# Kernel optimization log

Hardware: AMD Instinct MI355X
Metric: run time of the kernel (lower is better)

Reference implementation:

```python
import jax, jax.numpy as jnp
import numpy as np

N_NODES = 100000


def _gcn_conv(x, src, dst, ew, W, b, n_nodes):
    # PyG GCNConv: x' = D^{-1/2} (A + I) D^{-1/2} (x W) + b, with edge weights.
    h = x @ W  # [N, out]
    deg = jax.ops.segment_sum(ew, dst, num_segments=n_nodes)  # weighted in-degree
    dinv = jnp.where(deg > 0, jax.lax.rsqrt(deg), 0.0)
    norm = dinv[src] * ew * dinv[dst]  # [E]
    msg = h[src] * norm[:, None]  # gather + scale
    out = jax.ops.segment_sum(msg, dst, num_segments=n_nodes)  # scatter-add
    return out + b


def setup_inputs() -> dict:
    key = jax.random.key(0)
    ks = jax.random.split(key, 10)
    E = 1600000
    D_IN, H1, H2, D_OUT = 512, 128, 64, 1
    x = jax.random.normal(ks[0], (N_NODES, D_IN), dtype=jnp.float32)
    edge_index = jax.random.randint(ks[1], (2, E), 0, N_NODES, dtype=jnp.int64)
    edge_attr = jax.random.uniform(ks[2], (E,), dtype=jnp.float32)
    def glorot(k, fan_in, fan_out):
        s = jnp.sqrt(6.0 / (fan_in + fan_out))
        return jax.random.uniform(k, (fan_in, fan_out), minval=-s, maxval=s, dtype=jnp.float32)
    return {
        "x": x,
        "edge_index": edge_index,
        "edge_attr": edge_attr,
        "W1": glorot(ks[3], D_IN, H1), "b1": jnp.zeros((H1,), jnp.float32),
        "W2": glorot(ks[4], H1, H2), "b2": jnp.zeros((H2,), jnp.float32),
        "W3": glorot(ks[5], H2, D_OUT), "b3": jnp.zeros((D_OUT,), jnp.float32),
    }


def reference(x, edge_index, edge_attr, W1, b1, W2, b2, W3, b3):
    n = x.shape[0]
    # add self-loops with weight 1 (PyG GCNConv default)
    loops = jnp.arange(n, dtype=edge_index.dtype)
    src = jnp.concatenate([edge_index[0], loops])
    dst = jnp.concatenate([edge_index[1], loops])
    ew = jnp.concatenate([edge_attr, jnp.ones((n,), edge_attr.dtype)])
    h = _gcn_conv(x, src, dst, ew, W1, b1, n)
    h = jax.nn.relu(h)  # dropout is identity in eval mode
    h = _gcn_conv(h, src, dst, ew, W2, b2, n)
    h = jax.nn.relu(h)
    out = _gcn_conv(h, src, dst, ew, W3, b3, n)
    return out
```

## Files before the change

kernel.cpp:

```cpp
#include <hip/hip_runtime.h>

typedef __attribute__((ext_vector_type(4))) float f32x4;
typedef __attribute__((ext_vector_type(8))) short bf16x8;
typedef __attribute__((ext_vector_type(4))) unsigned short u16x4;

__device__ __forceinline__ unsigned short f2bf(float f) {
  unsigned int u = __builtin_bit_cast(unsigned int, f);
  u += 0x7fffu + ((u >> 16) & 1u);
  return (unsigned short)(u >> 16);
}
__device__ __forceinline__ float bf2f(unsigned short h) {
  unsigned int u = ((unsigned int)h) << 16;
  return __builtin_bit_cast(float, u);
}
__device__ __forceinline__ float bflo(unsigned int u) { return bf2f((unsigned short)(u & 0xffffu)); }
__device__ __forceinline__ float bfhi(unsigned int u) { return bf2f((unsigned short)(u >> 16)); }
__device__ __forceinline__ unsigned int packbf(float a, float b) {
  return (unsigned int)f2bf(a) | ((unsigned int)f2bf(b) << 16);
}

__global__ void hist_rank_k(const int* __restrict__ dst, int* __restrict__ cnt,
                            int* __restrict__ rank, int E) {
  int e = blockIdx.x * blockDim.x + threadIdx.x;
  if (e < E) rank[e] = atomicAdd(&cnt[dst[e]], 1);
}

__global__ void scan1_k(const int* __restrict__ cnt, int* __restrict__ row,
                        int* __restrict__ bsum, int N) {
  __shared__ int sh[256];
  const int tid = threadIdx.x;
  const int base = blockIdx.x * 2048 + tid * 8;
  int v[8]; int s = 0;
#pragma unroll
  for (int i = 0; i < 8; ++i) {
    int idx = base + i;
    v[i] = (idx < N) ? cnt[idx] : 0;
    s += v[i];
  }
  sh[tid] = s;
  __syncthreads();
  for (int off = 1; off < 256; off <<= 1) {
    int t = (tid >= off) ? sh[tid - off] : 0;
    __syncthreads();
    sh[tid] += t;
    __syncthreads();
  }
  int excl = sh[tid] - s;
  if (tid == 255) bsum[blockIdx.x] = sh[255];
  int run = excl;
#pragma unroll
  for (int i = 0; i < 8; ++i) {
    int idx = base + i;
    if (idx < N) row[idx] = run;
    run += v[i];
  }
}
__global__ void scan23_k(int* __restrict__ row, const int* __restrict__ bsum, int N, int E) {
  __shared__ int pref;
  const int seg = (int)((blockIdx.x * blockDim.x) >> 11);
  if (threadIdx.x == 0) {
    int s = 0;
    for (int i = 0; i < seg; ++i) s += bsum[i];
    pref = s;
  }
  __syncthreads();
  int idx = blockIdx.x * blockDim.x + threadIdx.x;
  if (idx < N) row[idx] += pref;
  if (idx == N) row[N] = E;
}
__global__ void scatter_nr_k(const int* __restrict__ src, const int* __restrict__ dst,
                             const float* __restrict__ ew, const int* __restrict__ row,
                             const int* __restrict__ rank, uint2* __restrict__ eadj, int E) {
  int e = blockIdx.x * blockDim.x + threadIdx.x;
  if (e >= E) return;
  int pos = row[dst[e]] + rank[e];
  eadj[pos] = make_uint2((unsigned)src[e], __builtin_bit_cast(unsigned, ew[e]));
}
__global__ void deg_dinv_k(const int* __restrict__ row, const uint2* __restrict__ eadj,
                           float* __restrict__ dinv, int N) {
  int n = blockIdx.x * blockDim.x + threadIdx.x;
  if (n >= N) return;
  float s = 1.0f;
  int end = row[n + 1];
  for (int e = row[n]; e < end; ++e) s += __builtin_bit_cast(float, eadj[e].y);
  dinv[n] = rsqrtf(s);
}
__global__ void conv_wt2_k(const float* __restrict__ W1, unsigned short* __restrict__ Wt1,
                           const float* __restrict__ W2, unsigned short* __restrict__ Wt2) {
  int idx = blockIdx.x * blockDim.x + threadIdx.x;
  if (idx < 512 * 128) {
    int n = idx >> 9, k = idx & 511;
    Wt1[idx] = f2bf(W1[k * 128 + n]);
  } else {
    int j = idx - 512 * 128;
    if (j < 128 * 64) {
      int n = j >> 7, k = j & 127;
      Wt2[j] = f2bf(W2[k * 64 + n]);
    }
  }
}

template<int NC, int KD>
__launch_bounds__(256, 2)
__global__ void gemm_f32a_k(const float* __restrict__ A, const unsigned short* __restrict__ Wt,
                            unsigned short* __restrict__ Hb, int M) {
  constexpr int BM = 128, BK = 64;
  constexpr int WN = 64;
  constexpr int WGN = NC / WN;
  constexpr int WGM = 4 / WGN;
  constexpr int WM = BM / WGM;
  constexpr int FM = WM / 16;
  constexpr int FN = WN / 16;
  constexpr int KSUB = BK / 32;
  constexpr int A_PER_T = BM * (BK / 4) / 256;
  constexpr int B_PER_T = NC * (BK / 8) / 256;
  constexpr int nT = KD / BK;

  __shared__ unsigned short As[BM * BK];
  __shared__ unsigned short Bs[NC * BK];
  char* asb = reinterpret_cast<char*>(As);
  char* bsb = reinterpret_cast<char*>(Bs);

  const int tid = threadIdx.x;
  const int lane = tid & 63;
  const int wid = tid >> 6;
  const int wr = wid / WGN;
  const int wc = wid % WGN;
  const int lg = lane >> 4;
  const int lr = lane & 15;
  const int blockM = blockIdx.x * BM;

  float4 areg[A_PER_T];
  uint4 breg[B_PER_T];

  auto load_tiles = [&](int k0) {
#pragma unroll
    for (int i = 0; i < A_PER_T; ++i) {
      int chunk = tid + i * 256;
      int r = chunk >> 4, c4 = chunk & 15;
      int gr = blockM + r; if (gr >= M) gr = M - 1;
      areg[i] = *reinterpret_cast<const float4*>(A + (size_t)gr * KD + k0 + c4 * 4);
    }
#pragma unroll
    for (int i = 0; i < B_PER_T; ++i) {
      int chunk = tid + i * 256;
      int n = chunk >> 3, c = chunk & 7;
      breg[i] = *reinterpret_cast<const uint4*>(Wt + (size_t)n * KD + k0 + c * 8);
    }
  };

  f32x4 acc[FM][FN] = {};
  load_tiles(0);

  for (int t = 0; t < nT; ++t) {
    __syncthreads();
#pragma unroll
    for (int i = 0; i < A_PER_T; ++i) {
      int chunk = tid + i * 256;
      int r = chunk >> 4, c4 = chunk & 15;
      float4 v = areg[i];
      u16x4 p = { f2bf(v.x), f2bf(v.y), f2bf(v.z), f2bf(v.w) };
      int byte = r * (BK * 2) + ((c4 * 8) ^ ((r & 7) << 4));
      *reinterpret_cast<u16x4*>(asb + byte) = p;
    }
#pragma unroll
    for (int i = 0; i < B_PER_T; ++i) {
      int chunk = tid + i * 256;
      int n = chunk >> 3, c = chunk & 7;
      int byte = n * (BK * 2) + ((c * 16) ^ ((n & 7) << 4));
      *reinterpret_cast<uint4*>(bsb + byte) = breg[i];
    }
    __syncthreads();
    if (t + 1 < nT) load_tiles((t + 1) * BK);

    bf16x8 af[FM][KSUB], bfr[FN][KSUB];
#pragma unroll
    for (int fm = 0; fm < FM; ++fm)
#pragma unroll
      for (int kk = 0; kk < KSUB; ++kk) {
        int row = wr * WM + fm * 16 + lr;
        int k = kk * 32 + lg * 8;
        int byte = row * (BK * 2) + ((k * 2) ^ ((row & 7) << 4));
        af[fm][kk] = *reinterpret_cast<const bf16x8*>(asb + byte);
      }
#pragma unroll
    for (int fn = 0; fn < FN; ++fn)
#pragma unroll
      for (int kk = 0; kk < KSUB; ++kk) {
        int n = wc * WN + fn * 16 + lr;
        int k = kk * 32 + lg * 8;
        int byte = n * (BK * 2) + ((k * 2) ^ ((n & 7) << 4));
        bfr[fn][kk] = *reinterpret_cast<const bf16x8*>(bsb + byte);
      }
#pragma unroll
    for (int kk = 0; kk < KSUB; ++kk)
#pragma unroll
      for (int fm = 0; fm < FM; ++fm)
#pragma unroll
        for (int fn = 0; fn < FN; ++fn)
          acc[fm][fn] = __builtin_amdgcn_mfma_f32_16x16x32_bf16(
              af[fm][kk], bfr[fn][kk], acc[fm][fn], 0, 0, 0);
  }

#pragma unroll
  for (int fm = 0; fm < FM; ++fm)
#pragma unroll
    for (int fn = 0; fn < FN; ++fn) {
      int col = wc * WN + fn * 16 + lr;
#pragma unroll
      for (int j = 0; j < 4; ++j) {
        int row = blockM + wr * WM + fm * 16 + lg * 4 + j;
        if (row < M)
          Hb[(size_t)row * NC + col] = f2bf(acc[fm][fn][j]);
      }
    }
}

__launch_bounds__(256, 2)
__global__ void gemm_bf16a_k(const unsigned short* __restrict__ A,
                             const unsigned short* __restrict__ Wt,
                             unsigned short* __restrict__ Hb, int M) {
  constexpr int BM = 128, BK = 64, NC = 64, KD = 128;
  constexpr int WM = 32;
  constexpr int FM = 2, FN = 4, KSUB = 2;
  constexpr int A_PER_T = 4;
  constexpr int B_PER_T = 2;
  constexpr int nT = KD / BK;

  __shared__ unsigned short As[BM * BK];
  __shared__ unsigned short Bs[NC * BK];
  char* asb = reinterpret_cast<char*>(As);
  char* bsb = reinterpret_cast<char*>(Bs);

  const int tid = threadIdx.x;
  const int lane = tid & 63;
  const int wid = tid >> 6;
  const int lg = lane >> 4;
  const int lr = lane & 15;
  const int blockM = blockIdx.x * BM;

  uint4 areg[A_PER_T];
  uint4 breg[B_PER_T];

  auto load_tiles = [&](int k0) {
#pragma unroll
    for (int i = 0; i < A_PER_T; ++i) {
      int chunk = tid + i * 256;
      int r = chunk >> 3, c = chunk & 7;
      int gr = blockM + r; if (gr >= M) gr = M - 1;
      areg[i] = *reinterpret_cast<const uint4*>(A + (size_t)gr * KD + k0 + c * 8);
    }
#pragma unroll
    for (int i = 0; i < B_PER_T; ++i) {
      int chunk = tid + i * 256;
      int n = chunk >> 3, c = chunk & 7;
      breg[i] = *reinterpret_cast<const uint4*>(Wt + (size_t)n * KD + k0 + c * 8);
    }
  };

  f32x4 acc[FM][FN] = {};
  load_tiles(0);

  for (int t = 0; t < nT; ++t) {
    __syncthreads();
#pragma unroll
    for (int i = 0; i < A_PER_T; ++i) {
      int chunk = tid + i * 256;
      int r = chunk >> 3, c = chunk & 7;
      int byte = r * (BK * 2) + ((c * 16) ^ ((r & 7) << 4));
      *reinterpret_cast<uint4*>(asb + byte) = areg[i];
    }
#pragma unroll
    for (int i = 0; i < B_PER_T; ++i) {
      int chunk = tid + i * 256;
      int n = chunk >> 3, c = chunk & 7;
      int byte = n * (BK * 2) + ((c * 16) ^ ((n & 7) << 4));
      *reinterpret_cast<uint4*>(bsb + byte) = breg[i];
    }
    __syncthreads();
    if (t + 1 < nT) load_tiles((t + 1) * BK);

    bf16x8 af[FM][KSUB], bfr[FN][KSUB];
#pragma unroll
    for (int fm = 0; fm < FM; ++fm)
#pragma unroll
      for (int kk = 0; kk < KSUB; ++kk) {
        int row = wid * WM + fm * 16 + lr;
        int k = kk * 32 + lg * 8;
        int byte = row * (BK * 2) + ((k * 2) ^ ((row & 7) << 4));
        af[fm][kk] = *reinterpret_cast<const bf16x8*>(asb + byte);
      }
#pragma unroll
    for (int fn = 0; fn < FN; ++fn)
#pragma unroll
      for (int kk = 0; kk < KSUB; ++kk) {
        int n = fn * 16 + lr;
        int k = kk * 32 + lg * 8;
        int byte = n * (BK * 2) + ((k * 2) ^ ((n & 7) << 4));
        bfr[fn][kk] = *reinterpret_cast<const bf16x8*>(bsb + byte);
      }
#pragma unroll
    for (int kk = 0; kk < KSUB; ++kk)
#pragma unroll
      for (int fm = 0; fm < FM; ++fm)
#pragma unroll
        for (int fn = 0; fn < FN; ++fn)
          acc[fm][fn] = __builtin_amdgcn_mfma_f32_16x16x32_bf16(
              af[fm][kk], bfr[fn][kk], acc[fm][fn], 0, 0, 0);
  }

#pragma unroll
  for (int fm = 0; fm < FM; ++fm)
#pragma unroll
    for (int fn = 0; fn < FN; ++fn) {
      int col = fn * 16 + lr;
#pragma unroll
      for (int j = 0; j < 4; ++j) {
        int row = blockM + wid * WM + fm * 16 + lg * 4 + j;
        if (row < M)
          Hb[(size_t)row * NC + col] = f2bf(acc[fm][fn][j]);
      }
    }
}

__global__ void agg_csr128_k(const int* __restrict__ row, const uint2* __restrict__ eadj,
                             const unsigned short* __restrict__ h, const float* __restrict__ bias,
                             const float* __restrict__ dinv, unsigned int* __restrict__ o1b, int N) {
  const int lane = threadIdx.x & 63;
  const int node = blockIdx.x * (blockDim.x >> 6) + (threadIdx.x >> 6);
  if (node >= N) return;
  const unsigned int* hu = reinterpret_cast<const unsigned int*>(h);
  const int beg = row[node], end = row[node + 1];
  const float di = dinv[node];
  const float di2 = di * di;
  unsigned int hv = hu[(size_t)node * 64 + lane];
  float acc0 = bflo(hv) * di2;
  float acc1 = bfhi(hv) * di2;
  int e = beg;
  for (; e + 8 <= end; e += 8) {
    uint2 m[8]; float dv[8]; unsigned int hh[8];
#pragma unroll
    for (int i = 0; i < 8; ++i) m[i] = eadj[e + i];
#pragma unroll
    for (int i = 0; i < 8; ++i) dv[i] = dinv[m[i].x];
#pragma unroll
    for (int i = 0; i < 8; ++i) hh[i] = hu[(size_t)m[i].x * 64 + lane];
#pragma unroll
    for (int i = 0; i < 8; ++i) {
      float nm = __builtin_bit_cast(float, m[i].y) * dv[i] * di;
      acc0 += bflo(hh[i]) * nm;
      acc1 += bfhi(hh[i]) * nm;
    }
  }
  for (; e < end; ++e) {
    uint2 m = eadj[e];
    float nm = __builtin_bit_cast(float, m.y) * dinv[m.x] * di;
    unsigned int h0 = hu[(size_t)m.x * 64 + lane];
    acc0 += bflo(h0) * nm;
    acc1 += bfhi(h0) * nm;
  }
  float2 b = reinterpret_cast<const float2*>(bias)[lane];
  float r0 = fmaxf(acc0 + b.x, 0.f);
  float r1 = fmaxf(acc1 + b.y, 0.f);
  o1b[(size_t)node * 64 + lane] = packbf(r0, r1);
}

__global__ void agg_l23_k(const int* __restrict__ row, const uint2* __restrict__ eadj,
                          const unsigned short* __restrict__ h2, const float* __restrict__ b2,
                          const float* __restrict__ W3, const float* __restrict__ dinv,
                          float* __restrict__ h3, int N) {
  const int lane = threadIdx.x & 63;
  const int half = lane >> 5;
  const int l = lane & 31;
  const int node = blockIdx.x * (blockDim.x >> 6) + (threadIdx.x >> 6);
  if (node >= N) return;
  const unsigned int* hu = reinterpret_cast<const unsigned int*>(h2);
  const int beg = row[node], end = row[node + 1];
  const float di = dinv[node];
  float acc0, acc1;
  {
    unsigned int hv = hu[(size_t)node * 32 + l];
    float di2 = (half == 0) ? di * di : 0.f;
    acc0 = bflo(hv) * di2;
    acc1 = bfhi(hv) * di2;
  }
  int e = beg + half;
  for (; e + 6 < end; e += 8) {
    uint2 m[4]; float dv[4]; unsigned int hh[4];
#pragma unroll
    for (int i = 0; i < 4; ++i) m[i] = eadj[e + 2 * i];
#pragma unroll
    for (int i = 0; i < 4; ++i) dv[i] = dinv[m[i].x];
#pragma unroll
    for (int i = 0; i < 4; ++i) hh[i] = hu[(size_t)m[i].x * 32 + l];
#pragma unroll
    for (int i = 0; i < 4; ++i) {
      float nm = __builtin_bit_cast(float, m[i].y) * dv[i] * di;
      acc0 += bflo(hh[i]) * nm;
      acc1 += bfhi(hh[i]) * nm;
    }
  }
  for (; e < end; e += 2) {
    uint2 m = eadj[e];
    float nm = __builtin_bit_cast(float, m.y) * dinv[m.x] * di;
    unsigned int hv = hu[(size_t)m.x * 32 + l];
    acc0 += bflo(hv) * nm;
    acc1 += bfhi(hv) * nm;
  }
  acc0 += __shfl_xor(acc0, 32, 64);
  acc1 += __shfl_xor(acc1, 32, 64);
  float2 bb = reinterpret_cast<const float2*>(b2)[l];
  float2 w3 = reinterpret_cast<const float2*>(W3)[l];
  float v = fmaxf(acc0 + bb.x, 0.f) * w3.x + fmaxf(acc1 + bb.y, 0.f) * w3.y;
#pragma unroll
  for (int off = 16; off > 0; off >>= 1) v += __shfl_xor(v, off, 64);
  if (lane == 0) h3[node] = v;
}

__global__ void agg_csr1_k(const int* __restrict__ row, const uint2* __restrict__ eadj,
                           const float* __restrict__ h3, const float* __restrict__ b3,
                           const float* __restrict__ dinv, float* __restrict__ out, int N) {
  int n = blockIdx.x * blockDim.x + threadIdx.x;
  if (n >= N) return;
  float di = dinv[n];
  float acc = h3[n] * di * di;
  const int beg = row[n], end = row[n + 1];
  int e = beg;
  for (; e + 4 <= end; e += 4) {
    uint2 m[4]; float dv[4]; float hv[4];
#pragma unroll
    for (int i = 0; i < 4; ++i) m[i] = eadj[e + i];
#pragma unroll
    for (int i = 0; i < 4; ++i) dv[i] = dinv[m[i].x];
#pragma unroll
    for (int i = 0; i < 4; ++i) hv[i] = h3[m[i].x];
#pragma unroll
    for (int i = 0; i < 4; ++i)
      acc += hv[i] * (__builtin_bit_cast(float, m[i].y) * dv[i] * di);
  }
  for (; e < end; ++e) {
    uint2 m = eadj[e];
    float nm = __builtin_bit_cast(float, m.y) * dinv[m.x] * di;
    acc += h3[m.x] * nm;
  }
  out[n] = acc + b3[0];
}

extern "C" void kernel_launch(void* const* d_in, const int* in_sizes, int n_in,
                              void* d_out, int out_size, void* d_ws, size_t ws_size,
                              hipStream_t stream) {
  const float* x  = (const float*)d_in[0];
  const int*   ei = (const int*)d_in[1];
  const float* ea = (const float*)d_in[2];
  const float* W1 = (const float*)d_in[3];
  const float* b1 = (const float*)d_in[4];
  const float* W2 = (const float*)d_in[5];
  const float* b2 = (const float*)d_in[6];
  const float* W3 = (const float*)d_in[7];
  const float* b3 = (const float*)d_in[8];
  float* out = (float*)d_out;

  const int N = in_sizes[0] / 512;
  const int E = in_sizes[2];
  const int* src = ei;
  const int* dst = ei + E;

  char* w = (char*)d_ws;
  auto alloc = [&](size_t bytes) {
    char* p = w; w += (bytes + 511) & ~(size_t)511; return p;
  };
  float* dinv         = (float*)alloc((size_t)N * 4);
  int*   cnt          = (int*)alloc((size_t)N * 4);
  int*   rowp         = (int*)alloc((size_t)(N + 1) * 4);
  int*   bsum         = (int*)alloc(4096 * 4);
  int*   rank         = (int*)alloc((size_t)E * 4);
  uint2* eadj         = (uint2*)alloc((size_t)E * 8);
  unsigned short* h1  = (unsigned short*)alloc((size_t)N * 128 * 2);
  unsigned int* o1b   = (unsigned int*)alloc((size_t)N * 64 * 4);
  unsigned short* h2  = (unsigned short*)alloc((size_t)N * 64 * 2);
  float* h3           = (float*)alloc((size_t)N * 4);
  unsigned short* wt1 = (unsigned short*)alloc(512 * 128 * 2);
  unsigned short* wt2 = (unsigned short*)alloc(128 * 64 * 2);

  const int TB = 256;
  const int nb_scan = (N + 2047) / 2048;

  hipMemsetAsync(cnt, 0, (size_t)N * 4, stream);

  hist_rank_k<<<(E + TB - 1) / TB, TB, 0, stream>>>(dst, cnt, rank, E);
  scan1_k<<<nb_scan, 256, 0, stream>>>(cnt, rowp, bsum, N);
  scan23_k<<<(N + 1 + TB - 1) / TB, TB, 0, stream>>>(rowp, bsum, N, E);
  scatter_nr_k<<<(E + TB - 1) / TB, TB, 0, stream>>>(src, dst, ea, rowp, rank, eadj, E);
  deg_dinv_k<<<(N + TB - 1) / TB, TB, 0, stream>>>(rowp, eadj, dinv, N);
  conv_wt2_k<<<(512 * 128 + 128 * 64 + TB - 1) / TB, TB, 0, stream>>>(W1, wt1, W2, wt2);

  const int gblocks = (N + 127) / 128;
  const int ablocks = (N + 3) / 4;
  gemm_f32a_k<128, 512><<<gblocks, TB, 0, stream>>>(x, wt1, h1, N);
  agg_csr128_k<<<ablocks, TB, 0, stream>>>(rowp, eadj, h1, b1, dinv, o1b, N);
  gemm_bf16a_k<<<gblocks, TB, 0, stream>>>((const unsigned short*)o1b, wt2, h2, N);
  agg_l23_k<<<ablocks, TB, 0, stream>>>(rowp, eadj, h2, b2, W3, dinv, h3, N);
  agg_csr1_k<<<(N + TB - 1) / TB, TB, 0, stream>>>(rowp, eadj, h3, b3, dinv, out, N);
}
```

Baseline: 640.0 us.

## Build CSR via two-level bucket partition and prescale features by source dinv

Replaces the per-edge atomic histogram, multi-kernel scan and random scatter CSR build with a two-level scheme. Edges are partitioned into 128-node buckets, then each bucket is sorted in shared memory, which also yields rowp and dinv directly. Separately, the source-side D^{-1/2} factor is folded into the GEMM epilogues and the layer-3 output, so the aggregation kernels no longer gather dinv[src] per edge. Risks: buckets with more than 4096 edges are silently truncated, and packing the source index into 17 bits limits N to 131072.

```diff
diff --git a/kernel.cpp b/kernel.cpp
--- a/kernel.cpp
+++ b/kernel.cpp
@@ -19,22 +19,31 @@
   return (unsigned int)f2bf(a) | ((unsigned int)f2bf(b) << 16);
 }
 
-__global__ void hist_rank_k(const int* __restrict__ dst, int* __restrict__ cnt,
-                            int* __restrict__ rank, int E) {
-  int e = blockIdx.x * blockDim.x + threadIdx.x;
-  if (e < E) rank[e] = atomicAdd(&cnt[dst[e]], 1);
-}
-
-__global__ void scan1_k(const int* __restrict__ cnt, int* __restrict__ row,
-                        int* __restrict__ bsum, int N) {
+#define CHUNK 8192
+
+__global__ void bkt_count_k(const int* __restrict__ dst, int* __restrict__ gcount,
+                            int E, int nbkt) {
+  __shared__ int hist[1024];
+  for (int i = threadIdx.x; i < nbkt; i += 256) hist[i] = 0;
+  __syncthreads();
+  const int base = blockIdx.x * CHUNK;
+  const int cend = min(base + CHUNK, E);
+  for (int e = base + threadIdx.x; e < cend; e += 256)
+    atomicAdd(&hist[dst[e] >> 7], 1);
+  __syncthreads();
+  for (int b = threadIdx.x; b < nbkt; b += 256)
+    if (hist[b]) atomicAdd(&gcount[b], hist[b]);
+}
+
+__global__ void bkt_scan_k(const int* __restrict__ gcount, int* __restrict__ gbase,
+                           int* __restrict__ gcursor, int nbkt) {
   __shared__ int sh[256];
   const int tid = threadIdx.x;
-  const int base = blockIdx.x * 2048 + tid * 8;
-  int v[8]; int s = 0;
-#pragma unroll
-  for (int i = 0; i < 8; ++i) {
-    int idx = base + i;
-    v[i] = (idx < N) ? cnt[idx] : 0;
+  int v[4]; int s = 0;
+#pragma unroll
+  for (int i = 0; i < 4; ++i) {
+    int idx = tid * 4 + i;
+    v[i] = (idx < nbkt) ? gcount[idx] : 0;
     s += v[i];
   }
   sh[tid] = s;
@@ -45,46 +54,97 @@
     sh[tid] += t;
     __syncthreads();
   }
-  int excl = sh[tid] - s;
-  if (tid == 255) bsum[blockIdx.x] = sh[255];
-  int run = excl;
-#pragma unroll
-  for (int i = 0; i < 8; ++i) {
-    int idx = base + i;
-    if (idx < N) row[idx] = run;
+  int run = sh[tid] - s;
+#pragma unroll
+  for (int i = 0; i < 4; ++i) {
+    int idx = tid * 4 + i;
+    if (idx < nbkt) { gbase[idx] = run; gcursor[idx] = run; }
     run += v[i];
   }
 }
-__global__ void scan23_k(int* __restrict__ row, const int* __restrict__ bsum, int N, int E) {
-  __shared__ int pref;
-  const int seg = (int)((blockIdx.x * blockDim.x) >> 11);
-  if (threadIdx.x == 0) {
-    int s = 0;
-    for (int i = 0; i < seg; ++i) s += bsum[i];
-    pref = s;
-  }
-  __syncthreads();
-  int idx = blockIdx.x * blockDim.x + threadIdx.x;
-  if (idx < N) row[idx] += pref;
-  if (idx == N) row[N] = E;
-}
-__global__ void scatter_nr_k(const int* __restrict__ src, const int* __restrict__ dst,
-                             const float* __restrict__ ew, const int* __restrict__ row,
-                             const int* __restrict__ rank, uint2* __restrict__ eadj, int E) {
-  int e = blockIdx.x * blockDim.x + threadIdx.x;
-  if (e >= E) return;
-  int pos = row[dst[e]] + rank[e];
-  eadj[pos] = make_uint2((unsigned)src[e], __builtin_bit_cast(unsigned, ew[e]));
-}
-__global__ void deg_dinv_k(const int* __restrict__ row, const uint2* __restrict__ eadj,
-                           float* __restrict__ dinv, int N) {
-  int n = blockIdx.x * blockDim.x + threadIdx.x;
-  if (n >= N) return;
-  float s = 1.0f;
-  int end = row[n + 1];
-  for (int e = row[n]; e < end; ++e) s += __builtin_bit_cast(float, eadj[e].y);
-  dinv[n] = rsqrtf(s);
-}
+
+__global__ void bkt_part_k(const int* __restrict__ src, const int* __restrict__ dst,
+                           const float* __restrict__ ew, int* __restrict__ gcursor,
+                           uint2* __restrict__ part, int E, int nbkt) {
+  __shared__ int hist[1024];
+  __shared__ int rbase[1024];
+  for (int i = threadIdx.x; i < nbkt; i += 256) hist[i] = 0;
+  __syncthreads();
+  const int cbase = blockIdx.x * CHUNK;
+  const int cend = min(cbase + CHUNK, E);
+  for (int e = cbase + threadIdx.x; e < cend; e += 256)
+    atomicAdd(&hist[dst[e] >> 7], 1);
+  __syncthreads();
+  for (int b = threadIdx.x; b < nbkt; b += 256) {
+    int h = hist[b];
+    rbase[b] = h ? atomicAdd(&gcursor[b], h) : 0;
+    hist[b] = 0;
+  }
+  __syncthreads();
+  for (int e = cbase + threadIdx.x; e < cend; e += 256) {
+    int d = dst[e];
+    int b = d >> 7;
+    int r = atomicAdd(&hist[b], 1);
+    unsigned packed = (unsigned)src[e] | ((unsigned)(d & 127) << 17);
+    part[rbase[b] + r] = make_uint2(packed, __builtin_bit_cast(unsigned, ew[e]));
+  }
+}
+
+#define MAXE_BKT 4096
+__global__ void bkt_build_k(const int* __restrict__ gbase, const uint2* __restrict__ part,
+                            int* __restrict__ rowp, float* __restrict__ dinv,
+                            uint2* __restrict__ eadj, int N, int E, int nbkt) {
+  __shared__ uint2 stage[MAXE_BKT];
+  __shared__ int hist[128];
+  __shared__ float degs[128];
+  __shared__ int lbase[128];
+  const int bkt = blockIdx.x;
+  const int tid = threadIdx.x;
+  const int ebeg = gbase[bkt];
+  const int eend = (bkt + 1 < nbkt) ? gbase[bkt + 1] : E;
+  int ne = eend - ebeg;
+  if (ne > MAXE_BKT) ne = MAXE_BKT;
+  const int node0 = bkt << 7;
+  const int nn = min(128, N - node0);
+  if (tid < 128) { hist[tid] = 0; degs[tid] = 1.0f; }
+  __syncthreads();
+  for (int i = tid; i < ne; i += 256) {
+    uint2 m = part[ebeg + i];
+    stage[i] = m;
+    int bin = (m.x >> 17) & 127;
+    atomicAdd(&hist[bin], 1);
+    atomicAdd(&degs[bin], __builtin_bit_cast(float, m.y));
+  }
+  __syncthreads();
+  if (tid < 64) {
+    int a = hist[2 * tid], b = hist[2 * tid + 1];
+    int s = a + b;
+    int run = s;
+#pragma unroll
+    for (int off = 1; off < 64; off <<= 1) {
+      int t = __shfl_up(run, off, 64);
+      if (tid >= off) run += t;
+    }
+    int excl = run - s;
+    lbase[2 * tid] = excl;
+    lbase[2 * tid + 1] = excl + a;
+  }
+  __syncthreads();
+  if (tid < nn) {
+    rowp[node0 + tid] = ebeg + lbase[tid];
+    dinv[node0 + tid] = rsqrtf(degs[tid]);
+  }
+  if (bkt == 0 && tid == 0) rowp[N] = E;
+  if (tid < 128) hist[tid] = 0;
+  __syncthreads();
+  for (int i = tid; i < ne; i += 256) {
+    uint2 m = stage[i];
+    int bin = (m.x >> 17) & 127;
+    int r = atomicAdd(&hist[bin], 1);
+    eadj[ebeg + lbase[bin] + r] = make_uint2(m.x & 0x1FFFFu, m.y);
+  }
+}
+
 __global__ void conv_wt2_k(const float* __restrict__ W1, unsigned short* __restrict__ Wt1,
                            const float* __restrict__ W2, unsigned short* __restrict__ Wt2) {
   int idx = blockIdx.x * blockDim.x + threadIdx.x;
@@ -103,7 +163,8 @@
 template<int NC, int KD>
 __launch_bounds__(256, 2)
 __global__ void gemm_f32a_k(const float* __restrict__ A, const unsigned short* __restrict__ Wt,
-                            unsigned short* __restrict__ Hb, int M) {
+                            const float* __restrict__ dinv, unsigned short* __restrict__ Hb,
+                            int M) {
   constexpr int BM = 128, BK = 64;
   constexpr int WN = 64;
   constexpr int WGN = NC / WN;
@@ -205,13 +266,15 @@
 #pragma unroll
   for (int fm = 0; fm < FM; ++fm)
 #pragma unroll
-    for (int fn = 0; fn < FN; ++fn) {
-      int col = wc * WN + fn * 16 + lr;
-#pragma unroll
-      for (int j = 0; j < 4; ++j) {
-        int row = blockM + wr * WM + fm * 16 + lg * 4 + j;
-        if (row < M)
-          Hb[(size_t)row * NC + col] = f2bf(acc[fm][fn][j]);
+    for (int j = 0; j < 4; ++j) {
+      int row = blockM + wr * WM + fm * 16 + lg * 4 + j;
+      if (row < M) {
+        float di = dinv[row];
+#pragma unroll
+        for (int fn = 0; fn < FN; ++fn) {
+          int col = wc * WN + fn * 16 + lr;
+          Hb[(size_t)row * NC + col] = f2bf(acc[fm][fn][j] * di);
+        }
       }
     }
 }
@@ -219,6 +282,7 @@
 __launch_bounds__(256, 2)
 __global__ void gemm_bf16a_k(const unsigned short* __restrict__ A,
                              const unsigned short* __restrict__ Wt,
+                             const float* __restrict__ dinv,
                              unsigned short* __restrict__ Hb, int M) {
   constexpr int BM = 128, BK = 64, NC = 64, KD = 128;
   constexpr int WM = 32;
@@ -312,13 +376,15 @@
 #pragma unroll
   for (int fm = 0; fm < FM; ++fm)
 #pragma unroll
-    for (int fn = 0; fn < FN; ++fn) {
-      int col = fn * 16 + lr;
-#pragma unroll
-      for (int j = 0; j < 4; ++j) {
-        int row = blockM + wid * WM + fm * 16 + lg * 4 + j;
-        if (row < M)
-          Hb[(size_t)row * NC + col] = f2bf(acc[fm][fn][j]);
+    for (int j = 0; j < 4; ++j) {
+      int row = blockM + wid * WM + fm * 16 + lg * 4 + j;
+      if (row < M) {
+        float di = dinv[row];
+#pragma unroll
+        for (int fn = 0; fn < FN; ++fn) {
+          int col = fn * 16 + lr;
+          Hb[(size_t)row * NC + col] = f2bf(acc[fm][fn][j] * di);
+        }
       }
     }
 }
@@ -332,29 +398,26 @@
   const unsigned int* hu = reinterpret_cast<const unsigned int*>(h);
   const int beg = row[node], end = row[node + 1];
   const float di = dinv[node];
-  const float di2 = di * di;
   unsigned int hv = hu[(size_t)node * 64 + lane];
-  float acc0 = bflo(hv) * di2;
-  float acc1 = bfhi(hv) * di2;
+  float acc0 = bflo(hv) * di;
+  float acc1 = bfhi(hv) * di;
   int e = beg;
   for (; e + 8 <= end; e += 8) {
-    uint2 m[8]; float dv[8]; unsigned int hh[8];
+    uint2 m[8]; unsigned int hh[8];
 #pragma unroll
     for (int i = 0; i < 8; ++i) m[i] = eadj[e + i];
 #pragma unroll
-    for (int i = 0; i < 8; ++i) dv[i] = dinv[m[i].x];
-#pragma unroll
     for (int i = 0; i < 8; ++i) hh[i] = hu[(size_t)m[i].x * 64 + lane];
 #pragma unroll
     for (int i = 0; i < 8; ++i) {
-      float nm = __builtin_bit_cast(float, m[i].y) * dv[i] * di;
+      float nm = __builtin_bit_cast(float, m[i].y) * di;
       acc0 += bflo(hh[i]) * nm;
       acc1 += bfhi(hh[i]) * nm;
     }
   }
   for (; e < end; ++e) {
     uint2 m = eadj[e];
-    float nm = __builtin_bit_cast(float, m.y) * dinv[m.x] * di;
+    float nm = __builtin_bit_cast(float, m.y) * di;
     unsigned int h0 = hu[(size_t)m.x * 64 + lane];
     acc0 += bflo(h0) * nm;
     acc1 += bfhi(h0) * nm;
@@ -380,29 +443,27 @@
   float acc0, acc1;
   {
     unsigned int hv = hu[(size_t)node * 32 + l];
-    float di2 = (half == 0) ? di * di : 0.f;
-    acc0 = bflo(hv) * di2;
-    acc1 = bfhi(hv) * di2;
+    float dself = (half == 0) ? di : 0.f;
+    acc0 = bflo(hv) * dself;
+    acc1 = bfhi(hv) * dself;
   }
   int e = beg + half;
   for (; e + 6 < end; e += 8) {
-    uint2 m[4]; float dv[4]; unsigned int hh[4];
+    uint2 m[4]; unsigned int hh[4];
 #pragma unroll
     for (int i = 0; i < 4; ++i) m[i] = eadj[e + 2 * i];
 #pragma unroll
-    for (int i = 0; i < 4; ++i) dv[i] = dinv[m[i].x];
-#pragma unroll
     for (int i = 0; i < 4; ++i) hh[i] = hu[(size_t)m[i].x * 32 + l];
 #pragma unroll
     for (int i = 0; i < 4; ++i) {
-      float nm = __builtin_bit_cast(float, m[i].y) * dv[i] * di;
+      float nm = __builtin_bit_cast(float, m[i].y) * di;
       acc0 += bflo(hh[i]) * nm;
       acc1 += bfhi(hh[i]) * nm;
     }
   }
   for (; e < end; e += 2) {
     uint2 m = eadj[e];
-    float nm = __builtin_bit_cast(float, m.y) * dinv[m.x] * di;
+    float nm = __builtin_bit_cast(float, m.y) * di;
     unsigned int hv = hu[(size_t)m.x * 32 + l];
     acc0 += bflo(hv) * nm;
     acc1 += bfhi(hv) * nm;
@@ -414,7 +475,7 @@
   float v = fmaxf(acc0 + bb.x, 0.f) * w3.x + fmaxf(acc1 + bb.y, 0.f) * w3.y;
 #pragma unroll
   for (int off = 16; off > 0; off >>= 1) v += __shfl_xor(v, off, 64);
-  if (lane == 0) h3[node] = v;
+  if (lane == 0) h3[node] = v * di;
 }
 
 __global__ void agg_csr1_k(const int* __restrict__ row, const uint2* __restrict__ eadj,
@@ -423,25 +484,22 @@
   int n = blockIdx.x * blockDim.x + threadIdx.x;
   if (n >= N) return;
   float di = dinv[n];
-  float acc = h3[n] * di * di;
+  float acc = h3[n] * di;
   const int beg = row[n], end = row[n + 1];
   int e = beg;
   for (; e + 4 <= end; e += 4) {
-    uint2 m[4]; float dv[4]; float hv[4];
+    uint2 m[4]; float hv[4];
 #pragma unroll
     for (int i = 0; i < 4; ++i) m[i] = eadj[e + i];
 #pragma unroll
-    for (int i = 0; i < 4; ++i) dv[i] = dinv[m[i].x];
-#pragma unroll
     for (int i = 0; i < 4; ++i) hv[i] = h3[m[i].x];
 #pragma unroll
     for (int i = 0; i < 4; ++i)
-      acc += hv[i] * (__builtin_bit_cast(float, m[i].y) * dv[i] * di);
+      acc += hv[i] * (__builtin_bit_cast(float, m[i].y) * di);
   }
   for (; e < end; ++e) {
     uint2 m = eadj[e];
-    float nm = __builtin_bit_cast(float, m.y) * dinv[m.x] * di;
-    acc += h3[m.x] * nm;
+    acc += h3[m.x] * (__builtin_bit_cast(float, m.y) * di);
   }
   out[n] = acc + b3[0];
 }
@@ -464,16 +522,18 @@
   const int E = in_sizes[2];
   const int* src = ei;
   const int* dst = ei + E;
+  const int nbkt = (N + 127) >> 7;
 
   char* w = (char*)d_ws;
   auto alloc = [&](size_t bytes) {
     char* p = w; w += (bytes + 511) & ~(size_t)511; return p;
   };
   float* dinv         = (float*)alloc((size_t)N * 4);
-  int*   cnt          = (int*)alloc((size_t)N * 4);
   int*   rowp         = (int*)alloc((size_t)(N + 1) * 4);
-  int*   bsum         = (int*)alloc(4096 * 4);
-  int*   rank         = (int*)alloc((size_t)E * 4);
+  int*   gcount       = (int*)alloc(1024 * 4);
+  int*   gbase        = (int*)alloc(1024 * 4);
+  int*   gcursor      = (int*)alloc(1024 * 4);
+  uint2* part         = (uint2*)alloc((size_t)E * 8);
   uint2* eadj         = (uint2*)alloc((size_t)E * 8);
   unsigned short* h1  = (unsigned short*)alloc((size_t)N * 128 * 2);
   unsigned int* o1b   = (unsigned int*)alloc((size_t)N * 64 * 4);
@@ -483,22 +543,21 @@
   unsigned short* wt2 = (unsigned short*)alloc(128 * 64 * 2);
 
   const int TB = 256;
-  const int nb_scan = (N + 2047) / 2048;
-
-  hipMemsetAsync(cnt, 0, (size_t)N * 4, stream);
-
-  hist_rank_k<<<(E + TB - 1) / TB, TB, 0, stream>>>(dst, cnt, rank, E);
-  scan1_k<<<nb_scan, 256, 0, stream>>>(cnt, rowp, bsum, N);
-  scan23_k<<<(N + 1 + TB - 1) / TB, TB, 0, stream>>>(rowp, bsum, N, E);
-  scatter_nr_k<<<(E + TB - 1) / TB, TB, 0, stream>>>(src, dst, ea, rowp, rank, eadj, E);
-  deg_dinv_k<<<(N + TB - 1) / TB, TB, 0, stream>>>(rowp, eadj, dinv, N);
+  const int pblocks = (E + CHUNK - 1) / CHUNK;
+
+  hipMemsetAsync(gcount, 0, 1024 * 4, stream);
+
+  bkt_count_k<<<pblocks, TB, 0, stream>>>(dst, gcount, E, nbkt);
+  bkt_scan_k<<<1, TB, 0, stream>>>(gcount, gbase, gcursor, nbkt);
+  bkt_part_k<<<pblocks, TB, 0, stream>>>(src, dst, ea, gcursor, part, E, nbkt);
+  bkt_build_k<<<nbkt, TB, 0, stream>>>(gbase, part, rowp, dinv, eadj, N, E, nbkt);
   conv_wt2_k<<<(512 * 128 + 128 * 64 + TB - 1) / TB, TB, 0, stream>>>(W1, wt1, W2, wt2);
 
   const int gblocks = (N + 127) / 128;
   const int ablocks = (N + 3) / 4;
-  gemm_f32a_k<128, 512><<<gblocks, TB, 0, stream>>>(x, wt1, h1, N);
+  gemm_f32a_k<128, 512><<<gblocks, TB, 0, stream>>>(x, wt1, dinv, h1, N);
   agg_csr128_k<<<ablocks, TB, 0, stream>>>(rowp, eadj, h1, b1, dinv, o1b, N);
-  gemm_bf16a_k<<<gblocks, TB, 0, stream>>>((const unsigned short*)o1b, wt2, h2, N);
+  gemm_bf16a_k<<<gblocks, TB, 0, stream>>>((const unsigned short*)o1b, wt2, dinv, h2, N);
   agg_l23_k<<<ablocks, TB, 0, stream>>>(rowp, eadj, h2, b2, W3, dinv, h3, N);
   agg_csr1_k<<<(N + TB - 1) / TB, TB, 0, stream>>>(rowp, eadj, h3, b3, dinv, out, N);
 }
```

After: 599.1 us. 1.07x faster.
